# Kernel optimization log

Hardware: AMD Instinct MI355X
Metric: run time of the kernel (lower is better)

## Reference

```python
import jax, jax.numpy as jnp
import numpy as np

B, H_RES, W_RES, C, WS, SHIFT, NH = 32, 64, 64, 256, 8, 4, 8
N = WS * WS              # tokens per window
HD = C // NH             # head dim
HID = 4 * C              # mlp hidden
CPB_HID = 512            # relative-position MLP hidden


def _rel_index():
    coords = np.stack(np.meshgrid(np.arange(WS), np.arange(WS), indexing='ij'))  # [2,WS,WS]
    cf = coords.reshape(2, -1)
    rel = (cf[:, :, None] - cf[:, None, :]).transpose(1, 2, 0).astype(np.int64)  # [n,n,2]
    rel[..., 0] += WS - 1
    rel[..., 1] += WS - 1
    rel[..., 0] *= 2 * WS - 1
    return rel.sum(-1)  # [n,n] indices into (2WS-1)^2 table

REL_INDEX = _rel_index()


def _attn_mask():
    img = np.zeros((H_RES, W_RES))
    slices = (slice(0, -WS), slice(-WS, -SHIFT), slice(-SHIFT, None))
    cnt = 0
    for hs in slices:
        for ws_ in slices:
            img[hs, ws_] = cnt
            cnt += 1
    mw = img.reshape(H_RES // WS, WS, W_RES // WS, WS).transpose(0, 2, 1, 3).reshape(-1, N)
    am = mw[:, None, :] - mw[:, :, None]  # [nw,n,n]
    return np.where(am != 0, -100.0, 0.0).astype(np.float32)

ATTN_MASK = _attn_mask()


def _cpb_table():
    r = np.arange(-(WS - 1), WS, dtype=np.float32)
    t = np.stack(np.meshgrid(r, r, indexing='ij'), axis=-1)[None]  # [1,2WS-1,2WS-1,2]
    t = t / (WS - 1) * 8.0
    t = np.sign(t) * np.log2(np.abs(t) + 1.0) / np.log2(8.0)
    return t.astype(np.float32)

CPB_TABLE = _cpb_table()


def setup_inputs() -> dict:
    key = jax.random.key(0)
    ks = jax.random.split(key, 10)
    s = 0.02
    return {
        'x': jax.random.normal(ks[0], (B, H_RES * W_RES, C), jnp.float32),
        'qkv_w': jax.random.normal(ks[1], (3 * C, C), jnp.float32) * s,
        'q_bias': jnp.zeros((C,), jnp.float32),
        'v_bias': jnp.zeros((C,), jnp.float32),
        'logit_scale': jnp.full((NH, 1, 1), jnp.log(10.0), jnp.float32),
        'cpb_w1': jax.random.normal(ks[2], (CPB_HID, 2), jnp.float32) * s,
        'cpb_b1': jnp.zeros((CPB_HID,), jnp.float32),
        'cpb_w2': jax.random.normal(ks[3], (NH, CPB_HID), jnp.float32) * s,
        'proj_w': jax.random.normal(ks[4], (C, C), jnp.float32) * s,
        'proj_b': jnp.zeros((C,), jnp.float32),
        'norm1_g': jnp.ones((C,), jnp.float32),
        'norm1_b': jnp.zeros((C,), jnp.float32),
        'norm2_g': jnp.ones((C,), jnp.float32),
        'norm2_b': jnp.zeros((C,), jnp.float32),
        'fc1_w': jax.random.normal(ks[5], (HID, C), jnp.float32) * s,
        'fc1_b': jnp.zeros((HID,), jnp.float32),
        'fc2_w': jax.random.normal(ks[6], (C, HID), jnp.float32) * s,
        'fc2_b': jnp.zeros((C,), jnp.float32),
    }


def _layernorm(x, g, b, eps=1e-5):
    m = jnp.mean(x, axis=-1, keepdims=True)
    v = jnp.mean(jnp.square(x - m), axis=-1, keepdims=True)
    return (x - m) * jax.lax.rsqrt(v + eps) * g + b


def _l2norm(x, eps=1e-12):
    n = jnp.sqrt(jnp.sum(jnp.square(x), axis=-1, keepdims=True))
    return x / jnp.maximum(n, eps)


def reference(x, qkv_w, q_bias, v_bias, logit_scale, cpb_w1, cpb_b1, cpb_w2,
              proj_w, proj_b, norm1_g, norm1_b, norm2_g, norm2_b,
              fc1_w, fc1_b, fc2_w, fc2_b):
    shortcut = x
    xv = x.reshape(B, H_RES, W_RES, C)
    # cyclic shift
    sx = jnp.roll(xv, (-SHIFT, -SHIFT), axis=(1, 2))
    # window partition -> [B*nw, N, C]
    win = sx.reshape(B, H_RES // WS, WS, W_RES // WS, WS, C)
    win = win.transpose(0, 1, 3, 2, 4, 5).reshape(-1, N, C)

    # qkv with zero k-bias
    qkv_bias = jnp.concatenate([q_bias, jnp.zeros_like(v_bias), v_bias])
    qkv = win @ qkv_w.T + qkv_bias
    qkv = qkv.reshape(-1, N, 3, NH, HD).transpose(2, 0, 3, 1, 4)  # [3,Bw,NH,N,HD]
    q, k, v = qkv[0], qkv[1], qkv[2]

    # cosine attention with clamped learnable temperature
    attn = jnp.einsum('whnd,whmd->whnm', _l2norm(q), _l2norm(k))
    scale = jnp.exp(jnp.minimum(logit_scale, jnp.log(100.0)))  # [NH,1,1]
    attn = attn * scale

    # continuous relative position bias via MLP
    table = jnp.asarray(CPB_TABLE)  # [1,2WS-1,2WS-1,2]
    hmid = jax.nn.relu(table @ cpb_w1.T + cpb_b1)
    bias_table = (hmid @ cpb_w2.T).reshape(-1, NH)  # [(2WS-1)^2, NH]
    rpb = bias_table[jnp.asarray(REL_INDEX).reshape(-1)].reshape(N, N, NH)
    rpb = jax.nn.sigmoid(rpb.transpose(2, 0, 1)) * 16.0  # [NH,N,N]
    attn = attn + rpb[None]

    # shift mask
    mask = jnp.asarray(ATTN_MASK)  # [nw,N,N]
    nw = mask.shape[0]
    attn = attn.reshape(-1, nw, NH, N, N) + mask[None, :, None]
    attn = attn.reshape(-1, NH, N, N)
    attn = jax.nn.softmax(attn, axis=-1)

    out = jnp.einsum('whnm,whmd->whnd', attn, v).transpose(0, 2, 1, 3).reshape(-1, N, C)
    out = out @ proj_w.T + proj_b

    # window reverse + reverse shift
    out = out.reshape(B, H_RES // WS, W_RES // WS, WS, WS, C)
    out = out.transpose(0, 1, 3, 2, 4, 5).reshape(B, H_RES, W_RES, C)
    out = jnp.roll(out, (SHIFT, SHIFT), axis=(1, 2)).reshape(B, H_RES * W_RES, C)

    # post-norm residual (Swin v2 style)
    x1 = shortcut + _layernorm(out, norm1_g, norm1_b)
    mlp_out = jax.nn.gelu(x1 @ fc1_w.T + fc1_b, approximate=False) @ fc2_w.T + fc2_b
    x2 = x1 + _layernorm(mlp_out, norm2_g, norm2_b)
    return x2
```

## Files before the change

### kernel.cpp

```cpp
#include <hip/hip_runtime.h>

typedef unsigned short u16;
typedef unsigned int u32;
typedef __attribute__((ext_vector_type(8))) short bf16x8;
typedef __attribute__((ext_vector_type(4))) float f32x4;

#define CC_    256
#define NHD_   8
#define NT_    64
#define HD_    32
#define HID_   1024
#define CPBH_  512
#define BW_    2048
#define TOK_   131072
#define SHIFT_ 4

__device__ __forceinline__ int region9(int ph, int pw) {
  return (ph < 56 ? 0 : (ph < 60 ? 3 : 6)) + (pw < 56 ? 0 : (pw < 60 ? 1 : 2));
}
__device__ __forceinline__ float dot32(const float* qr, const float* krow) {
  float d0 = 0.f, d1 = 0.f, d2 = 0.f, d3 = 0.f;
#pragma unroll
  for (int d = 0; d < HD_; d += 4) {
    float4 kk = *reinterpret_cast<const float4*>(krow + d);
    d0 += qr[d] * kk.x; d1 += qr[d + 1] * kk.y;
    d2 += qr[d + 2] * kk.z; d3 += qr[d + 3] * kk.w;
  }
  return (d0 + d1) + (d2 + d3);
}

__device__ __forceinline__ u16 f2bf(float f) {
  u32 u = __builtin_bit_cast(u32, f);
  u = (u + 0x7FFFu + ((u >> 16) & 1u)) >> 16;
  return (u16)u;
}

__device__ __forceinline__ void split4(float4 f, uint2& hi, uint2& lo) {
  u16 h0 = f2bf(f.x), h1 = f2bf(f.y), h2 = f2bf(f.z), h3 = f2bf(f.w);
  float r0 = f.x - __builtin_bit_cast(float, (u32)h0 << 16);
  float r1 = f.y - __builtin_bit_cast(float, (u32)h1 << 16);
  float r2 = f.z - __builtin_bit_cast(float, (u32)h2 << 16);
  float r3 = f.w - __builtin_bit_cast(float, (u32)h3 << 16);
  hi = make_uint2((u32)h0 | ((u32)h1 << 16), (u32)h2 | ((u32)h3 << 16));
  lo = make_uint2((u32)f2bf(r0) | ((u32)f2bf(r1) << 16),
                  (u32)f2bf(r2) | ((u32)f2bf(r3) << 16));
}

__global__ void cpb_kernel(const float* __restrict__ w1, const float* __restrict__ b1,
                           const float* __restrict__ w2, float* __restrict__ bias_table) {
  __shared__ float hid[CPBH_];
  int p = blockIdx.x;
  int k = threadIdx.x;
  int hi = p / 15, wi = p % 15;
  float a0 = (float)(hi - 7) / 7.0f * 8.0f;
  float a1 = (float)(wi - 7) / 7.0f * 8.0f;
  float t0 = (a0 == 0.0f) ? 0.0f : copysignf(log2f(fabsf(a0) + 1.0f) / 3.0f, a0);
  float t1 = (a1 == 0.0f) ? 0.0f : copysignf(log2f(fabsf(a1) + 1.0f) / 3.0f, a1);
  float h = t0 * w1[2 * k] + t1 * w1[2 * k + 1] + b1[k];
  hid[k] = fmaxf(h, 0.0f);
  __syncthreads();
  if (k < NHD_) {
    float s = 0.0f;
    for (int j = 0; j < CPBH_; j++) s += hid[j] * w2[k * CPBH_ + j];
    bias_table[p * NHD_ + k] = s;
  }
}

__global__ void rpb_kernel(const float* __restrict__ bias_table, float* __restrict__ rpb) {
  int h = blockIdx.x >> 6;
  int i = blockIdx.x & 63;
  int j = threadIdx.x;
  int dih = (i >> 3) - (j >> 3) + 7;
  int diw = (i & 7) - (j & 7) + 7;
  float v = bias_table[(dih * 15 + diw) * NHD_ + h];
  rpb[(((h << 6) + i) << 6) + j] = 16.0f / (1.0f + expf(-v));
}

__global__ void convw_kernel(const float* __restrict__ w, u16* __restrict__ o, int n) {
  int i = blockIdx.x * 256 + threadIdx.x;
  if (i < n) o[i] = f2bf(w[i]);
}

__global__ void convsplit_kernel(const float* __restrict__ w, u16* __restrict__ hi,
                                 u16* __restrict__ lo, int n) {
  int i = blockIdx.x * 256 + threadIdx.x;
  if (i < n) {
    float v = w[i];
    u16 h = f2bf(v);
    hi[i] = h;
    lo[i] = f2bf(v - __builtin_bit_cast(float, (u32)h << 16));
  }
}

__global__ __launch_bounds__(512) void qkv_mfma_kernel(
    const float* __restrict__ x,
    const u16* __restrict__ wh_, const u16* __restrict__ wl_,
    const float* __restrict__ qb, const float* __restrict__ vb,
    float* __restrict__ qo, float* __restrict__ ko, float* __restrict__ vo, int w0) {
  __shared__ u16 xh[64 * 256];
  __shared__ u16 xl[64 * 256];
  int tid = threadIdx.x;
  int lane = tid & 63, wid = tid >> 6;
  int lr = lane & 15, lk = lane >> 4;
  int wl2 = blockIdx.x;
  int w = w0 + wl2;
  int b = w >> 6, win = w & 63, wwh = win >> 3, www = win & 7;

#pragma unroll
  for (int i = 0; i < 8; i++) {
    int idx = tid + i * 512;
    int n = idx >> 6, c4 = idx & 63;
    int sh = wwh * 8 + (n >> 3), sw = www * 8 + (n & 7);
    int hh = (sh + SHIFT_) & 63, wc = (sw + SHIFT_) & 63;
    float4 f = *reinterpret_cast<const float4*>(
        x + ((size_t)((b << 12) + (hh << 6) + wc)) * CC_ + c4 * 4);
    uint2 hi, lo; split4(f, hi, lo);
    int u = c4 >> 1;
    int off16 = n * 256 + ((u ^ (n & 7)) << 3) + ((c4 & 1) << 2);
    *reinterpret_cast<uint2*>(&xh[off16]) = hi;
    *reinterpret_cast<uint2*>(&xl[off16]) = lo;
  }
  __syncthreads();

  f32x4 acc[4][6];
#pragma unroll
  for (int m = 0; m < 4; m++)
#pragma unroll
    for (int nf = 0; nf < 6; nf++) acc[m][nf] = (f32x4){0.f, 0.f, 0.f, 0.f};

  for (int k0 = 0; k0 < CC_; k0 += 32) {
    int u0 = (k0 >> 3) + lk;
    bf16x8 ah[4], al[4];
#pragma unroll
    for (int m = 0; m < 4; m++) {
      int row = m * 16 + lr;
      int off16 = row * 256 + ((u0 ^ (row & 7)) << 3);
      ah[m] = *reinterpret_cast<const bf16x8*>(&xh[off16]);
      al[m] = *reinterpret_cast<const bf16x8*>(&xl[off16]);
    }
#pragma unroll
    for (int nf = 0; nf < 6; nf++) {
      int col = wid * 96 + nf * 16 + lr;
      size_t wo = (size_t)col * CC_ + k0 + lk * 8;
      bf16x8 bh = *reinterpret_cast<const bf16x8*>(wh_ + wo);
      bf16x8 bl = *reinterpret_cast<const bf16x8*>(wl_ + wo);
#pragma unroll
      for (int m = 0; m < 4; m++) {
        acc[m][nf] = __builtin_amdgcn_mfma_f32_16x16x32_bf16(ah[m], bh, acc[m][nf], 0, 0, 0);
        acc[m][nf] = __builtin_amdgcn_mfma_f32_16x16x32_bf16(al[m], bh, acc[m][nf], 0, 0, 0);
        acc[m][nf] = __builtin_amdgcn_mfma_f32_16x16x32_bf16(ah[m], bl, acc[m][nf], 0, 0, 0);
      }
    }
  }

#pragma unroll
  for (int nf = 0; nf < 6; nf++) {
    int col = wid * 96 + nf * 16 + lr;
    int mat = col >> 8, cc = col & 255;
    float bias = (mat == 0) ? qb[cc] : ((mat == 2) ? vb[cc] : 0.f);
    float* dst = (mat == 0) ? qo : ((mat == 1) ? ko : vo);
    int hd = cc >> 5, d = cc & 31;
    float* dp = dst + ((size_t)(wl2 * NHD_ + hd) * NT_) * HD_ + d;
#pragma unroll
    for (int m = 0; m < 4; m++)
#pragma unroll
      for (int r = 0; r < 4; r++) {
        int n = m * 16 + lk * 4 + r;
        dp[(size_t)n * HD_] = acc[m][nf][r] + bias;
      }
  }
}

__global__ __launch_bounds__(64) void attn_kernel(
    const float* __restrict__ qq, const float* __restrict__ kk_, const float* __restrict__ vv_,
    const float* __restrict__ ls, const float* __restrict__ rpb, float* __restrict__ attn_out, int w0) {
  __shared__ float ks[NT_][HD_];
  __shared__ float vs[NT_][HD_];
  int bid = blockIdx.x;
  int wl = bid >> 3, h = bid & 7;
  int w = w0 + wl;
  int i = threadIdx.x;
  size_t base = (size_t)bid * (NT_ * HD_) + (size_t)i * HD_;

  float qr[HD_];
  float ss = 0.f;
#pragma unroll
  for (int d = 0; d < HD_; d += 4) {
    float4 f = *reinterpret_cast<const float4*>(qq + base + d);
    qr[d] = f.x; qr[d + 1] = f.y; qr[d + 2] = f.z; qr[d + 3] = f.w;
    ss += f.x * f.x + f.y * f.y + f.z * f.z + f.w * f.w;
  }
  float inv = 1.0f / fmaxf(sqrtf(ss), 1e-12f);
#pragma unroll
  for (int d = 0; d < HD_; d++) qr[d] *= inv;

  float kr[HD_]; ss = 0.f;
#pragma unroll
  for (int d = 0; d < HD_; d += 4) {
    float4 f = *reinterpret_cast<const float4*>(kk_ + base + d);
    kr[d] = f.x; kr[d + 1] = f.y; kr[d + 2] = f.z; kr[d + 3] = f.w;
    ss += f.x * f.x + f.y * f.y + f.z * f.z + f.w * f.w;
  }
  inv = 1.0f / fmaxf(sqrtf(ss), 1e-12f);
#pragma unroll
  for (int d = 0; d < HD_; d += 4) {
    float4 t; t.x = kr[d] * inv; t.y = kr[d + 1] * inv; t.z = kr[d + 2] * inv; t.w = kr[d + 3] * inv;
    *reinterpret_cast<float4*>(&ks[i][d]) = t;
  }
#pragma unroll
  for (int d = 0; d < HD_; d += 4) {
    float4 f = *reinterpret_cast<const float4*>(vv_ + base + d);
    *reinterpret_cast<float4*>(&vs[i][d]) = f;
  }
  __syncthreads();

  float scale = expf(fminf(ls[h], 4.605170185988091f));
  const float* rp = rpb + (((h << 6) + i) << 6);
  int win = w & 63, wh = win >> 3, ww = win & 7;
  int regi = region9(wh * 8 + (i >> 3), ww * 8 + (i & 7));

  float m = -1e30f, l = 0.f;
  for (int j = 0; j < NT_; j++) {
    float dot = dot32(qr, &ks[j][0]);
    int regj = region9(wh * 8 + (j >> 3), ww * 8 + (j & 7));
    float val = dot * scale + rp[j] + (regj == regi ? 0.f : -100.f);
    float nm = fmaxf(m, val);
    l = l * expf(m - nm) + expf(val - nm);
    m = nm;
  }
  float rl = 1.0f / l;

  float acc[HD_];
#pragma unroll
  for (int d = 0; d < HD_; d++) acc[d] = 0.f;
  for (int j = 0; j < NT_; j++) {
    float dot = dot32(qr, &ks[j][0]);
    int regj = region9(wh * 8 + (j >> 3), ww * 8 + (j & 7));
    float val = dot * scale + rp[j] + (regj == regi ? 0.f : -100.f);
    float p = expf(val - m) * rl;
#pragma unroll
    for (int d = 0; d < HD_; d += 4) {
      float4 vvv = *reinterpret_cast<const float4*>(&vs[j][d]);
      acc[d] += p * vvv.x; acc[d + 1] += p * vvv.y; acc[d + 2] += p * vvv.z; acc[d + 3] += p * vvv.w;
    }
  }
  float* op = attn_out + ((size_t)(wl * NT_ + i)) * CC_ + h * HD_;
#pragma unroll
  for (int d = 0; d < HD_; d += 4) {
    float4 t; t.x = acc[d]; t.y = acc[d + 1]; t.z = acc[d + 2]; t.w = acc[d + 3];
    *reinterpret_cast<float4*>(op + d) = t;
  }
}

__global__ __launch_bounds__(512) void proj_mfma_kernel(
    const float* __restrict__ attn_out,
    const u16* __restrict__ pwh, const u16* __restrict__ pwl, const float* __restrict__ pb,
    const float* __restrict__ g, const float* __restrict__ bb,
    const float* __restrict__ x, float* __restrict__ x1, int w0) {
  __shared__ union {
    struct { u16 ah[64 * 256]; u16 al[64 * 256]; } s;
    float po[64][CC_];
  } sm;
  int tid = threadIdx.x;
  int lane = tid & 63, wid = tid >> 6;
  int lr = lane & 15, lk = lane >> 4;
  int wl2 = blockIdx.x;
  int w = w0 + wl2;

#pragma unroll
  for (int i = 0; i < 8; i++) {
    int idx = tid + i * 512;
    int n = idx >> 6, c4 = idx & 63;
    float4 f = *reinterpret_cast<const float4*>(
        attn_out + ((size_t)(wl2 * NT_ + n)) * CC_ + c4 * 4);
    uint2 hi, lo; split4(f, hi, lo);
    int u = c4 >> 1;
    int off16 = n * 256 + ((u ^ (n & 7)) << 3) + ((c4 & 1) << 2);
    *reinterpret_cast<uint2*>(&sm.s.ah[off16]) = hi;
    *reinterpret_cast<uint2*>(&sm.s.al[off16]) = lo;
  }
  __syncthreads();

  f32x4 acc[4][2];
#pragma unroll
  for (int m = 0; m < 4; m++)
#pragma unroll
    for (int nf = 0; nf < 2; nf++) acc[m][nf] = (f32x4){0.f, 0.f, 0.f, 0.f};

  for (int k0 = 0; k0 < CC_; k0 += 32) {
    int u0 = (k0 >> 3) + lk;
    bf16x8 ah[4], al[4];
#pragma unroll
    for (int m = 0; m < 4; m++) {
      int row = m * 16 + lr;
      int off16 = row * 256 + ((u0 ^ (row & 7)) << 3);
      ah[m] = *reinterpret_cast<const bf16x8*>(&sm.s.ah[off16]);
      al[m] = *reinterpret_cast<const bf16x8*>(&sm.s.al[off16]);
    }
#pragma unroll
    for (int nf = 0; nf < 2; nf++) {
      int col = wid * 32 + nf * 16 + lr;
      size_t wo = (size_t)col * CC_ + k0 + lk * 8;
      bf16x8 bh = *reinterpret_cast<const bf16x8*>(pwh + wo);
      bf16x8 bl = *reinterpret_cast<const bf16x8*>(pwl + wo);
#pragma unroll
      for (int m = 0; m < 4; m++) {
        acc[m][nf] = __builtin_amdgcn_mfma_f32_16x16x32_bf16(ah[m], bh, acc[m][nf], 0, 0, 0);
        acc[m][nf] = __builtin_amdgcn_mfma_f32_16x16x32_bf16(al[m], bh, acc[m][nf], 0, 0, 0);
        acc[m][nf] = __builtin_amdgcn_mfma_f32_16x16x32_bf16(ah[m], bl, acc[m][nf], 0, 0, 0);
      }
    }
  }
  __syncthreads();

#pragma unroll
  for (int nf = 0; nf < 2; nf++) {
    int col = wid * 32 + nf * 16 + lr;
    float bv = pb[col];
#pragma unroll
    for (int m = 0; m < 4; m++)
#pragma unroll
      for (int r = 0; r < 4; r++)
        sm.po[m * 16 + lk * 4 + r][col] = acc[m][nf][r] + bv;
  }
  __syncthreads();

  int t = wid * 8 + (lane >> 3);
  int j8 = ((lane & 7) + (lane >> 3)) & 7;
  float4 pv[8];
  float sum = 0.f, sq = 0.f;
#pragma unroll
  for (int i = 0; i < 8; i++) {
    float4 v = *reinterpret_cast<const float4*>(&sm.po[t][j8 * 4 + i * 32]);
    pv[i] = v;
    sum += v.x + v.y + v.z + v.w;
    sq += v.x * v.x + v.y * v.y + v.z * v.z + v.w * v.w;
  }
#pragma unroll
  for (int off = 1; off < 8; off <<= 1) {
    sum += __shfl_xor(sum, off, 8);
    sq  += __shfl_xor(sq, off, 8);
  }
  float mean = sum * (1.0f / CC_);
  float var = sq * (1.0f / CC_) - mean * mean;
  float rs = rsqrtf(fmaxf(var, 0.0f) + 1e-5f);
  int b = w >> 6, win = w & 63, wwh = win >> 3, www = win & 7;
  int sh = wwh * 8 + (t >> 3), sw = www * 8 + (t & 7);
  int hh = (sh + SHIFT_) & 63, wc = (sw + SHIFT_) & 63;
  size_t tok = ((size_t)(b << 12)) + (hh << 6) + wc;
  const float* xrow = x + tok * CC_;
  float* orow = x1 + tok * CC_;
#pragma unroll
  for (int i = 0; i < 8; i++) {
    int c = j8 * 4 + i * 32;
    float4 xg = *reinterpret_cast<const float4*>(xrow + c);
    float4 gg = *reinterpret_cast<const float4*>(g + c);
    float4 bv = *reinterpret_cast<const float4*>(bb + c);
    float4 r;
    r.x = xg.x + (pv[i].x - mean) * rs * gg.x + bv.x;
    r.y = xg.y + (pv[i].y - mean) * rs * gg.y + bv.y;
    r.z = xg.z + (pv[i].z - mean) * rs * gg.z + bv.z;
    r.w = xg.w + (pv[i].w - mean) * rs * gg.w + bv.w;
    *reinterpret_cast<float4*>(orow + c) = r;
  }
}

#define BM_   64
#define PADX_ 264
#define PADH_ 136

__global__ __launch_bounds__(512) void mlp_mfma_kernel(
    const float* __restrict__ x1,
    const u16* __restrict__ w1bf, const float* __restrict__ b1,
    const u16* __restrict__ w2bf, const float* __restrict__ b2,
    const float* __restrict__ g, const float* __restrict__ bb,
    float* __restrict__ out) {
  __shared__ union {
    struct { u16 xs[BM_][PADX_]; u16 hid[BM_][PADH_]; } s;
    float po[BM_][CC_];
  } sm;

  int tid = threadIdx.x;
  int lane = tid & 63;
  int wid = tid >> 6;
  int wm = wid >> 2;
  int wn = wid & 3;
  int lr = lane & 15;
  int lk = lane >> 4;
  size_t t0 = (size_t)blockIdx.x * BM_;

#pragma unroll
  for (int i = 0; i < 8; i++) {
    int idx = tid + i * 512;
    int row = idx >> 6;
    int c4 = idx & 63;
    float4 f = *reinterpret_cast<const float4*>(x1 + (t0 + row) * CC_ + c4 * 4);
    u32 p0 = (u32)f2bf(f.x) | ((u32)f2bf(f.y) << 16);
    u32 p1 = (u32)f2bf(f.z) | ((u32)f2bf(f.w) << 16);
    *reinterpret_cast<uint2*>(&sm.s.xs[row][c4 * 4]) = make_uint2(p0, p1);
  }
  __syncthreads();

  f32x4 acc2[2][4];
#pragma unroll
  for (int mf = 0; mf < 2; mf++)
#pragma unroll
    for (int nf = 0; nf < 4; nf++) acc2[mf][nf] = (f32x4){0.f, 0.f, 0.f, 0.f};

  for (int ch = 0; ch < 8; ch++) {
    int h0 = ch * 128;
    f32x4 acc1[2][2];
#pragma unroll
    for (int mf = 0; mf < 2; mf++)
#pragma unroll
      for (int nf = 0; nf < 2; nf++) acc1[mf][nf] = (f32x4){0.f, 0.f, 0.f, 0.f};
#pragma unroll
    for (int k0 = 0; k0 < CC_; k0 += 32) {
      bf16x8 a0 = *reinterpret_cast<const bf16x8*>(&sm.s.xs[wm * 32 + lr][k0 + lk * 8]);
      bf16x8 a1 = *reinterpret_cast<const bf16x8*>(&sm.s.xs[wm * 32 + 16 + lr][k0 + lk * 8]);
      bf16x8 b0 = *reinterpret_cast<const bf16x8*>(w1bf + (size_t)(h0 + wn * 32 + lr) * CC_ + k0 + lk * 8);
      bf16x8 b1f = *reinterpret_cast<const bf16x8*>(w1bf + (size_t)(h0 + wn * 32 + 16 + lr) * CC_ + k0 + lk * 8);
      acc1[0][0] = __builtin_amdgcn_mfma_f32_16x16x32_bf16(a0, b0, acc1[0][0], 0, 0, 0);
      acc1[1][0] = __builtin_amdgcn_mfma_f32_16x16x32_bf16(a1, b0, acc1[1][0], 0, 0, 0);
      acc1[0][1] = __builtin_amdgcn_mfma_f32_16x16x32_bf16(a0, b1f, acc1[0][1], 0, 0, 0);
      acc1[1][1] = __builtin_amdgcn_mfma_f32_16x16x32_bf16(a1, b1f, acc1[1][1], 0, 0, 0);
    }
    __syncthreads();
    float bias0 = b1[h0 + wn * 32 + lr];
    float bias1 = b1[h0 + wn * 32 + 16 + lr];
#pragma unroll
    for (int mf = 0; mf < 2; mf++)
#pragma unroll
      for (int nf = 0; nf < 2; nf++) {
        float bv = nf ? bias1 : bias0;
        int col = wn * 32 + nf * 16 + lr;
#pragma unroll
        for (int r = 0; r < 4; r++) {
          int row = wm * 32 + mf * 16 + lk * 4 + r;
          float v = acc1[mf][nf][r] + bv;
          v = 0.5f * v * (1.0f + erff(v * 0.7071067811865475f));
          sm.s.hid[row][col] = f2bf(v);
        }
      }
    __syncthreads();
#pragma unroll
    for (int k0 = 0; k0 < 128; k0 += 32) {
      bf16x8 a0 = *reinterpret_cast<const bf16x8*>(&sm.s.hid[wm * 32 + lr][k0 + lk * 8]);
      bf16x8 a1 = *reinterpret_cast<const bf16x8*>(&sm.s.hid[wm * 32 + 16 + lr][k0 + lk * 8]);
#pragma unroll
      for (int nf = 0; nf < 4; nf++) {
        bf16x8 bf = *reinterpret_cast<const bf16x8*>(w2bf + (size_t)(wn * 64 + nf * 16 + lr) * HID_ + h0 + k0 + lk * 8);
        acc2[0][nf] = __builtin_amdgcn_mfma_f32_16x16x32_bf16(a0, bf, acc2[0][nf], 0, 0, 0);
        acc2[1][nf] = __builtin_amdgcn_mfma_f32_16x16x32_bf16(a1, bf, acc2[1][nf], 0, 0, 0);
      }
    }
  }
  __syncthreads();

#pragma unroll
  for (int mf = 0; mf < 2; mf++)
#pragma unroll
    for (int nf = 0; nf < 4; nf++) {
      int col = wn * 64 + nf * 16 + lr;
      float bv = b2[col];
#pragma unroll
      for (int r = 0; r < 4; r++) {
        int row = wm * 32 + mf * 16 + lk * 4 + r;
        sm.po[row][col] = acc2[mf][nf][r] + bv;
      }
    }
  __syncthreads();

  int t = wid * 8 + (lane >> 3);
  int j8 = ((lane & 7) + (lane >> 3)) & 7;
  float4 pv[8];
  float sum = 0.f, sq = 0.f;
#pragma unroll
  for (int i = 0; i < 8; i++) {
    float4 v = *reinterpret_cast<const float4*>(&sm.po[t][j8 * 4 + i * 32]);
    pv[i] = v;
    sum += v.x + v.y + v.z + v.w;
    sq += v.x * v.x + v.y * v.y + v.z * v.z + v.w * v.w;
  }
#pragma unroll
  for (int off = 1; off < 8; off <<= 1) {
    sum += __shfl_xor(sum, off, 8);
    sq  += __shfl_xor(sq, off, 8);
  }
  float mean = sum * (1.0f / CC_);
  float var = sq * (1.0f / CC_) - mean * mean;
  float rs = rsqrtf(fmaxf(var, 0.0f) + 1e-5f);
  const float* xrow = x1 + (t0 + t) * CC_;
  float* orow = out + (t0 + t) * CC_;
#pragma unroll
  for (int i = 0; i < 8; i++) {
    int c = j8 * 4 + i * 32;
    float4 xg = *reinterpret_cast<const float4*>(xrow + c);
    float4 gg = *reinterpret_cast<const float4*>(g + c);
    float4 bv = *reinterpret_cast<const float4*>(bb + c);
    float4 r;
    r.x = xg.x + (pv[i].x - mean) * rs * gg.x + bv.x;
    r.y = xg.y + (pv[i].y - mean) * rs * gg.y + bv.y;
    r.z = xg.z + (pv[i].z - mean) * rs * gg.z + bv.z;
    r.w = xg.w + (pv[i].w - mean) * rs * gg.w + bv.w;
    *reinterpret_cast<float4*>(orow + c) = r;
  }
}

extern "C" void kernel_launch(void* const* d_in, const int* in_sizes, int n_in,
                              void* d_out, int out_size, void* d_ws, size_t ws_size,
                              hipStream_t stream) {
  const float* x       = (const float*)d_in[0];
  const float* qkv_w   = (const float*)d_in[1];
  const float* q_bias  = (const float*)d_in[2];
  const float* v_bias  = (const float*)d_in[3];
  const float* logit_s = (const float*)d_in[4];
  const float* cpb_w1  = (const float*)d_in[5];
  const float* cpb_b1  = (const float*)d_in[6];
  const float* cpb_w2  = (const float*)d_in[7];
  const float* proj_w  = (const float*)d_in[8];
  const float* proj_b  = (const float*)d_in[9];
  const float* n1g     = (const float*)d_in[10];
  const float* n1b     = (const float*)d_in[11];
  const float* n2g     = (const float*)d_in[12];
  const float* n2b     = (const float*)d_in[13];
  const float* fc1_w   = (const float*)d_in[14];
  const float* fc1_b   = (const float*)d_in[15];
  const float* fc2_w   = (const float*)d_in[16];
  const float* fc2_b   = (const float*)d_in[17];
  float* out = (float*)d_out;
  char* ws = (char*)d_ws;

  u16* fc1bf = (u16*)(ws + 139264);
  u16* fc2bf = (u16*)(ws + 663552);
  u16* qwh   = (u16*)(ws + 1187840);
  u16* qwl   = (u16*)(ws + 1581056);
  u16* pwh   = (u16*)(ws + 1974272);
  u16* pwl   = (u16*)(ws + 2105344);
  const size_t OFF_CH = 2236416;
  const size_t ELEM_PER_WIN = (size_t)NHD_ * NT_ * HD_;
  const size_t PER_WIN_BYTES = 4 * ELEM_PER_WIN * 4;

  float* bias_table = (float*)(ws);
  float* rpb        = (float*)(ws + 8192);

  long long avail = (long long)ws_size - (long long)OFF_CH;
  long long ncw = avail / (long long)PER_WIN_BYTES;
  if (ncw < 1) ncw = 1;
  if (ncw > BW_) ncw = BW_;
  int nc = (int)ncw;

  float* qc = (float*)(ws + OFF_CH);
  float* kc = qc + (size_t)nc * ELEM_PER_WIN;
  float* vc = kc + (size_t)nc * ELEM_PER_WIN;
  float* ac = vc + (size_t)nc * ELEM_PER_WIN;

  cpb_kernel<<<225, 512, 0, stream>>>(cpb_w1, cpb_b1, cpb_w2, bias_table);
  rpb_kernel<<<NHD_ * NT_, 64, 0, stream>>>(bias_table, rpb);
  convw_kernel<<<1024, 256, 0, stream>>>(fc1_w, fc1bf, HID_ * CC_);
  convw_kernel<<<1024, 256, 0, stream>>>(fc2_w, fc2bf, CC_ * HID_);
  convsplit_kernel<<<768, 256, 0, stream>>>(qkv_w, qwh, qwl, 3 * CC_ * CC_);
  convsplit_kernel<<<256, 256, 0, stream>>>(proj_w, pwh, pwl, CC_ * CC_);

  for (int w0 = 0; w0 < BW_; w0 += nc) {
    int nw = (BW_ - w0 < nc) ? (BW_ - w0) : nc;
    qkv_mfma_kernel<<<nw, 512, 0, stream>>>(x, qwh, qwl, q_bias, v_bias, qc, kc, vc, w0);
    attn_kernel<<<nw * 8, 64, 0, stream>>>(qc, kc, vc, logit_s, rpb, ac, w0);
    proj_mfma_kernel<<<nw, 512, 0, stream>>>(ac, pwh, pwl, proj_b, n1g, n1b, x, out, w0);
  }
  mlp_mfma_kernel<<<TOK_ / BM_, 512, 0, stream>>>(out, fc1bf, fc1_b, fc2bf, fc2_b, n2g, n2b, out);
}
```

Measured before the change: 1.794 ms.

## Double-buffer MLP hidden tile and swizzle shared memory in fused MLP kernel

Restructures the fused FC1/GELU/FC2 MLP kernel. The hidden activation buffer is double-buffered, so FC1 for the next 128-wide chunk runs alongside FC2 of the current chunk, cutting two block barriers per chunk down to one. Padded shared-memory rows are replaced by an XOR swizzle. FC1 is computed transposed (weights as the A operand, tokens as B), so each lane writes four contiguous GELU outputs as one packed 8-byte store instead of scalar bf16 stores. The cost is more shared memory for the second hidden buffer and more index arithmetic.

```diff
diff --git a/kernel.cpp b/kernel.cpp
--- a/kernel.cpp
+++ b/kernel.cpp
@@ -366,8 +366,6 @@
 }
 
 #define BM_   64
-#define PADX_ 264
-#define PADH_ 136
 
 __global__ __launch_bounds__(512) void mlp_mfma_kernel(
     const float* __restrict__ x1,
@@ -376,17 +374,19 @@
     const float* __restrict__ g, const float* __restrict__ bb,
     float* __restrict__ out) {
   __shared__ union {
-    struct { u16 xs[BM_][PADX_]; u16 hid[BM_][PADH_]; } s;
+    struct { u16 xs[64 * 256]; u16 hid[2][64 * 128]; } s;
     float po[BM_][CC_];
   } sm;
 
   int tid = threadIdx.x;
   int lane = tid & 63;
   int wid = tid >> 6;
-  int wm = wid >> 2;
-  int wn = wid & 3;
   int lr = lane & 15;
   int lk = lane >> 4;
+  int whid = wid >> 1;
+  int wtok = wid & 1;
+  int wout = wid >> 1;
+  int wtk2 = wid & 1;
   size_t t0 = (size_t)blockIdx.x * BM_;
 
 #pragma unroll
@@ -397,9 +397,10 @@
     float4 f = *reinterpret_cast<const float4*>(x1 + (t0 + row) * CC_ + c4 * 4);
     u32 p0 = (u32)f2bf(f.x) | ((u32)f2bf(f.y) << 16);
     u32 p1 = (u32)f2bf(f.z) | ((u32)f2bf(f.w) << 16);
-    *reinterpret_cast<uint2*>(&sm.s.xs[row][c4 * 4]) = make_uint2(p0, p1);
-  }
-  __syncthreads();
+    int u = c4 >> 1;
+    int off16 = row * 256 + ((u ^ (row & 7)) << 3) + ((c4 & 1) << 2);
+    *reinterpret_cast<uint2*>(&sm.s.xs[off16]) = make_uint2(p0, p1);
+  }
 
   f32x4 acc2[2][4];
 #pragma unroll
@@ -407,65 +408,93 @@
 #pragma unroll
     for (int nf = 0; nf < 4; nf++) acc2[mf][nf] = (f32x4){0.f, 0.f, 0.f, 0.f};
 
-  for (int ch = 0; ch < 8; ch++) {
+  auto FC1 = [&](int ch) {
     int h0 = ch * 128;
     f32x4 acc1[2][2];
 #pragma unroll
-    for (int mf = 0; mf < 2; mf++)
-#pragma unroll
-      for (int nf = 0; nf < 2; nf++) acc1[mf][nf] = (f32x4){0.f, 0.f, 0.f, 0.f};
+    for (int hf = 0; hf < 2; hf++)
+#pragma unroll
+      for (int tf = 0; tf < 2; tf++) acc1[hf][tf] = (f32x4){0.f, 0.f, 0.f, 0.f};
 #pragma unroll
     for (int k0 = 0; k0 < CC_; k0 += 32) {
-      bf16x8 a0 = *reinterpret_cast<const bf16x8*>(&sm.s.xs[wm * 32 + lr][k0 + lk * 8]);
-      bf16x8 a1 = *reinterpret_cast<const bf16x8*>(&sm.s.xs[wm * 32 + 16 + lr][k0 + lk * 8]);
-      bf16x8 b0 = *reinterpret_cast<const bf16x8*>(w1bf + (size_t)(h0 + wn * 32 + lr) * CC_ + k0 + lk * 8);
-      bf16x8 b1f = *reinterpret_cast<const bf16x8*>(w1bf + (size_t)(h0 + wn * 32 + 16 + lr) * CC_ + k0 + lk * 8);
-      acc1[0][0] = __builtin_amdgcn_mfma_f32_16x16x32_bf16(a0, b0, acc1[0][0], 0, 0, 0);
-      acc1[1][0] = __builtin_amdgcn_mfma_f32_16x16x32_bf16(a1, b0, acc1[1][0], 0, 0, 0);
-      acc1[0][1] = __builtin_amdgcn_mfma_f32_16x16x32_bf16(a0, b1f, acc1[0][1], 0, 0, 0);
-      acc1[1][1] = __builtin_amdgcn_mfma_f32_16x16x32_bf16(a1, b1f, acc1[1][1], 0, 0, 0);
-    }
-    __syncthreads();
-    float bias0 = b1[h0 + wn * 32 + lr];
-    float bias1 = b1[h0 + wn * 32 + 16 + lr];
-#pragma unroll
-    for (int mf = 0; mf < 2; mf++)
-#pragma unroll
-      for (int nf = 0; nf < 2; nf++) {
-        float bv = nf ? bias1 : bias0;
-        int col = wn * 32 + nf * 16 + lr;
-#pragma unroll
-        for (int r = 0; r < 4; r++) {
-          int row = wm * 32 + mf * 16 + lk * 4 + r;
-          float v = acc1[mf][nf][r] + bv;
-          v = 0.5f * v * (1.0f + erff(v * 0.7071067811865475f));
-          sm.s.hid[row][col] = f2bf(v);
-        }
+      bf16x8 a0 = *reinterpret_cast<const bf16x8*>(
+          w1bf + (size_t)(h0 + whid * 32 + lr) * CC_ + k0 + lk * 8);
+      bf16x8 a1 = *reinterpret_cast<const bf16x8*>(
+          w1bf + (size_t)(h0 + whid * 32 + 16 + lr) * CC_ + k0 + lk * 8);
+      int u0 = (k0 >> 3) + lk;
+      int r0 = wtok * 32 + lr;
+      int r1 = wtok * 32 + 16 + lr;
+      bf16x8 bx0 = *reinterpret_cast<const bf16x8*>(&sm.s.xs[r0 * 256 + ((u0 ^ (r0 & 7)) << 3)]);
+      bf16x8 bx1 = *reinterpret_cast<const bf16x8*>(&sm.s.xs[r1 * 256 + ((u0 ^ (r1 & 7)) << 3)]);
+      acc1[0][0] = __builtin_amdgcn_mfma_f32_16x16x32_bf16(a0, bx0, acc1[0][0], 0, 0, 0);
+      acc1[0][1] = __builtin_amdgcn_mfma_f32_16x16x32_bf16(a0, bx1, acc1[0][1], 0, 0, 0);
+      acc1[1][0] = __builtin_amdgcn_mfma_f32_16x16x32_bf16(a1, bx0, acc1[1][0], 0, 0, 0);
+      acc1[1][1] = __builtin_amdgcn_mfma_f32_16x16x32_bf16(a1, bx1, acc1[1][1], 0, 0, 0);
+    }
+    u16* hb = &sm.s.hid[ch & 1][0];
+#pragma unroll
+    for (int hf = 0; hf < 2; hf++) {
+      float4 bq = *reinterpret_cast<const float4*>(b1 + h0 + whid * 32 + hf * 16 + lk * 4);
+      int col = whid * 32 + hf * 16 + lk * 4;
+      int u = col >> 3;
+      int half4 = (lk & 1) << 2;
+#pragma unroll
+      for (int tf = 0; tf < 2; tf++) {
+        int token = wtok * 32 + tf * 16 + lr;
+        float v0 = acc1[hf][tf][0] + bq.x;
+        float v1 = acc1[hf][tf][1] + bq.y;
+        float v2 = acc1[hf][tf][2] + bq.z;
+        float v3 = acc1[hf][tf][3] + bq.w;
+        v0 = 0.5f * v0 * (1.0f + erff(v0 * 0.7071067811865475f));
+        v1 = 0.5f * v1 * (1.0f + erff(v1 * 0.7071067811865475f));
+        v2 = 0.5f * v2 * (1.0f + erff(v2 * 0.7071067811865475f));
+        v3 = 0.5f * v3 * (1.0f + erff(v3 * 0.7071067811865475f));
+        u32 p0 = (u32)f2bf(v0) | ((u32)f2bf(v1) << 16);
+        u32 p1 = (u32)f2bf(v2) | ((u32)f2bf(v3) << 16);
+        int off16 = token * 128 + ((u ^ (token & 7)) << 3) + half4;
+        *reinterpret_cast<uint2*>(&hb[off16]) = make_uint2(p0, p1);
       }
-    __syncthreads();
-#pragma unroll
-    for (int k0 = 0; k0 < 128; k0 += 32) {
-      bf16x8 a0 = *reinterpret_cast<const bf16x8*>(&sm.s.hid[wm * 32 + lr][k0 + lk * 8]);
-      bf16x8 a1 = *reinterpret_cast<const bf16x8*>(&sm.s.hid[wm * 32 + 16 + lr][k0 + lk * 8]);
+    }
+  };
+
+  auto FC2 = [&](int ch) {
+    int h0 = ch * 128;
+    const u16* hb = &sm.s.hid[ch & 1][0];
+#pragma unroll
+    for (int kk = 0; kk < 128; kk += 32) {
+      int u0 = (kk >> 3) + lk;
+      int r0 = wtk2 * 32 + lr;
+      int r1 = wtk2 * 32 + 16 + lr;
+      bf16x8 a0 = *reinterpret_cast<const bf16x8*>(&hb[r0 * 128 + ((u0 ^ (r0 & 7)) << 3)]);
+      bf16x8 a1 = *reinterpret_cast<const bf16x8*>(&hb[r1 * 128 + ((u0 ^ (r1 & 7)) << 3)]);
 #pragma unroll
       for (int nf = 0; nf < 4; nf++) {
-        bf16x8 bf = *reinterpret_cast<const bf16x8*>(w2bf + (size_t)(wn * 64 + nf * 16 + lr) * HID_ + h0 + k0 + lk * 8);
+        bf16x8 bf = *reinterpret_cast<const bf16x8*>(
+            w2bf + (size_t)(wout * 64 + nf * 16 + lr) * HID_ + h0 + kk + lk * 8);
         acc2[0][nf] = __builtin_amdgcn_mfma_f32_16x16x32_bf16(a0, bf, acc2[0][nf], 0, 0, 0);
         acc2[1][nf] = __builtin_amdgcn_mfma_f32_16x16x32_bf16(a1, bf, acc2[1][nf], 0, 0, 0);
       }
     }
-  }
-  __syncthreads();
+  };
+
+  __syncthreads();
+  FC1(0);
+  __syncthreads();
+  for (int ch = 0; ch < 8; ch++) {
+    if (ch < 7) FC1(ch + 1);
+    FC2(ch);
+    __syncthreads();
+  }
 
 #pragma unroll
   for (int mf = 0; mf < 2; mf++)
 #pragma unroll
     for (int nf = 0; nf < 4; nf++) {
-      int col = wn * 64 + nf * 16 + lr;
+      int col = wout * 64 + nf * 16 + lr;
       float bv = b2[col];
 #pragma unroll
       for (int r = 0; r < 4; r++) {
-        int row = wm * 32 + mf * 16 + lk * 4 + r;
+        int row = wtk2 * 32 + mf * 16 + lk * 4 + r;
         sm.po[row][col] = acc2[mf][nf][r] + bv;
       }
     }
```

Result: faster. 1.673 ms (-6.7%).
